# Kernel optimization log

Hardware: AMD Instinct MI355X
Metric: run time of the kernel (lower is better)

Reference implementation:

```python
import jax, jax.numpy as jnp
import numpy as np

N = 100000        # nodes
E = 1600000       # directed edges (before self loops)
F = 128           # input node features
H1, H2, H3 = 64, 32, 16
G = 64            # graphs in batch
EPS = 1e-5
NEG_SLOPE = 0.2


def setup_inputs():
    key = jax.random.key(0)
    ks = jax.random.split(key, 16)
    def rn(k, shape, scale=1.0):
        return jax.random.normal(k, shape, dtype=jnp.float32) * scale
    inp = {}
    inp['x'] = rn(ks[0], (N, F))
    inp['edge_index'] = jax.random.randint(ks[1], (2, E), 0, N)
    inp['batch'] = jnp.sort(jax.random.randint(ks[2], (N,), 0, G))
    dims = [(F, H1), (H1, H2), (H2, H3)]
    i = 3
    for li, (fi, fo) in enumerate(dims, start=1):
        s = 1.0 / np.sqrt(fi)
        kk = jax.random.split(ks[i], 3)
        inp[f'Wl{li}'] = rn(kk[0], (fi, fo), s)
        inp[f'bl{li}'] = jnp.zeros((fo,), jnp.float32)
        inp[f'Wr{li}'] = rn(kk[1], (fi, fo), s)
        inp[f'br{li}'] = jnp.zeros((fo,), jnp.float32)
        inp[f'att{li}'] = rn(kk[2], (fo,), 1.0 / np.sqrt(fo))
        inp[f'bias{li}'] = jnp.zeros((fo,), jnp.float32)
        inp[f'gamma{li}'] = jnp.ones((fo,), jnp.float32)
        inp[f'beta{li}'] = jnp.zeros((fo,), jnp.float32)
        i += 1
    inp['linW'] = rn(ks[i], (H3, 1), 0.25)
    inp['linb'] = jnp.zeros((1,), jnp.float32)
    return inp


def _gatv2(x, Wl, bl, Wr, br, att, bias, src, dst):
    # PyG GATv2Conv, heads=1: e_ij = a^T LeakyReLU(Wl x_j + Wr x_i)
    xl = x @ Wl + bl                         # [N, H] source transform
    xr = x @ Wr + br                         # [N, H] target transform
    e = jax.nn.leaky_relu(xl[src] + xr[dst], NEG_SLOPE) @ att   # [E']
    # numerically stable segment softmax over incoming edges of dst
    emax = jax.ops.segment_max(e, dst, num_segments=N)
    w = jnp.exp(e - emax[dst])
    denom = jax.ops.segment_sum(w, dst, num_segments=N)
    alpha = w / (denom[dst] + 1e-16)         # [E']
    out = jax.ops.segment_sum(alpha[:, None] * xl[src], dst, num_segments=N)
    return out + bias


def _batchnorm(x, gamma, beta):
    mu = jnp.mean(x, axis=0)
    var = jnp.var(x, axis=0)
    return (x - mu) * jax.lax.rsqrt(var + EPS) * gamma + beta


def reference(x, edge_index, batch,
              Wl1, bl1, Wr1, br1, att1, bias1, gamma1, beta1,
              Wl2, bl2, Wr2, br2, att2, bias2, gamma2, beta2,
              Wl3, bl3, Wr3, br3, att3, bias3, gamma3, beta3,
              linW, linb):
    # add self loops once (PyG GATv2Conv default add_self_loops=True)
    loops = jnp.arange(N, dtype=edge_index.dtype)
    src = jnp.concatenate([edge_index[0], loops])
    dst = jnp.concatenate([edge_index[1], loops])

    h = _gatv2(x, Wl1, bl1, Wr1, br1, att1, bias1, src, dst)
    h = jax.nn.relu(_batchnorm(h, gamma1, beta1))
    h = _gatv2(h, Wl2, bl2, Wr2, br2, att2, bias2, src, dst)
    h = jax.nn.relu(_batchnorm(h, gamma2, beta2))
    h = _gatv2(h, Wl3, bl3, Wr3, br3, att3, bias3, src, dst)
    h = jax.nn.relu(_batchnorm(h, gamma3, beta3))

    # global mean pool over graphs
    sums = jax.ops.segment_sum(h, batch, num_segments=G)          # [G, 16]
    cnts = jax.ops.segment_sum(jnp.ones((N,), h.dtype), batch, num_segments=G)
    pooled = sums / jnp.maximum(cnts, 1.0)[:, None]
    return pooled @ linW + linb                                   # [G, 1]
```

## Files before the change

### kernel.cpp

```cpp
#include <hip/hip_runtime.h>
#include <hip/hip_bf16.h>


static constexpr int G_ = 64;

typedef short bfrag __attribute__((ext_vector_type(8)));
typedef float facc  __attribute__((ext_vector_type(4)));

__device__ __forceinline__ float bf2f(unsigned short u) {
  union { unsigned int i; float f; } c;
  c.i = ((unsigned int)u) << 16;
  return c.f;
}
__device__ __forceinline__ unsigned short f2bf(float f) {
  union { float f; unsigned int i; } c;
  c.f = f;
  unsigned int r = c.i + 0x7FFFu + ((c.i >> 16) & 1u);
  return (unsigned short)(r >> 16);
}

__global__ __launch_bounds__(256) void pack_all(
    const float* __restrict__ Wl1, const float* __restrict__ Wr1,
    const float* __restrict__ bl1, const float* __restrict__ br1,
    const float* __restrict__ Wl2, const float* __restrict__ Wr2,
    const float* __restrict__ bl2, const float* __restrict__ br2,
    const float* __restrict__ Wl3, const float* __restrict__ Wr3,
    const float* __restrict__ bl3, const float* __restrict__ br3,
    unsigned short* __restrict__ Wt1, float* __restrict__ bc1,
    unsigned short* __restrict__ Wt2, float* __restrict__ bc2,
    unsigned short* __restrict__ Wt3, float* __restrict__ bc3) {
  int i = blockIdx.x * 256 + threadIdx.x;
  if (i < 128 * 128) { int c = i >> 7, k = i & 127;
    Wt1[i] = f2bf((c < 64) ? Wl1[k * 64 + c] : Wr1[k * 64 + (c - 64)]); }
  if (i < 128) bc1[i] = (i < 64) ? bl1[i] : br1[i - 64];
  if (i < 64 * 64) { int c = i >> 6, k = i & 63;
    Wt2[i] = f2bf((c < 32) ? Wl2[k * 32 + c] : Wr2[k * 32 + (c - 32)]); }
  if (i < 64) bc2[i] = (i < 32) ? bl2[i] : br2[i - 32];
  if (i < 32 * 32) { int c = i >> 5, k = i & 31;
    Wt3[i] = f2bf((c < 16) ? Wl3[k * 16 + c] : Wr3[k * 16 + (c - 16)]); }
  if (i < 32) bc3[i] = (i < 16) ? bl3[i] : br3[i - 16];
}

__global__ __launch_bounds__(256) void edge_hist(
    const int* __restrict__ ei, int* __restrict__ deg, int E, int Etot, int N) {
  int p = blockIdx.x & 7;
  int q = blockIdx.x >> 3;
  int nbq = gridDim.x >> 3;
  float scale = 8.0f / (float)N;
  for (int i = q * 256 + threadIdx.x; i < Etot; i += nbq * 256) {
    int dst = (i < E) ? ei[E + i] : (i - E);
    int pp = min((int)((float)dst * scale), 7);
    if (pp == p) atomicAdd(&deg[dst], 1);
  }
}

__global__ __launch_bounds__(256) void scan1(
    const int* __restrict__ deg, int* __restrict__ part, int* __restrict__ bsums, int n) {
  __shared__ int ts[256];
  int t = threadIdx.x, b = blockIdx.x;
  int base = b * 1024 + t * 4;
  int d[4];
#pragma unroll
  for (int q = 0; q < 4; q++) d[q] = (base + q < n) ? deg[base + q] : 0;
  int s = d[0] + d[1] + d[2] + d[3];
  ts[t] = s;
  __syncthreads();
  for (int o = 1; o < 256; o <<= 1) {
    int v = (t >= o) ? ts[t - o] : 0;
    __syncthreads();
    ts[t] += v;
    __syncthreads();
  }
  int incl = ts[t];
  if (t == 255) bsums[b] = incl;
  int run = incl - s;
#pragma unroll
  for (int q = 0; q < 4; q++) {
    if (base + q < n) part[base + q] = run;
    run += d[q];
  }
}

__global__ void scan2(int* bsums, int nb) {
  __shared__ int s[256];
  int t = threadIdx.x;
  int v = (t < nb) ? bsums[t] : 0;
  s[t] = v;
  __syncthreads();
  for (int o = 1; o < 256; o <<= 1) {
    int u = (t >= o) ? s[t - o] : 0;
    __syncthreads();
    s[t] += u;
    __syncthreads();
  }
  if (t < nb) bsums[t] = s[t] - v;
}

__global__ __launch_bounds__(256) void scan3(
    int* __restrict__ rp, int* __restrict__ cur, const int* __restrict__ bsums,
    int n, int Etot) {
  int i = blockIdx.x * 256 + threadIdx.x;
  if (i < n) {
    int v = rp[i] + bsums[i >> 10];
    rp[i] = v; cur[i] = v;
  }
  if (i == 0) rp[n] = Etot;
}

__global__ __launch_bounds__(256) void scatter_edges(
    const int* __restrict__ ei, int* __restrict__ cur, int* __restrict__ ssrc,
    int E, int Etot, int N) {
  int p = blockIdx.x & 7;
  int q = blockIdx.x >> 3;
  int nbq = gridDim.x >> 3;
  float scale = 8.0f / (float)N;
  for (int i = q * 256 + threadIdx.x; i < Etot; i += nbq * 256) {
    int dst = (i < E) ? ei[E + i] : (i - E);
    int pp = min((int)((float)dst * scale), 7);
    if (pp != p) continue;
    int src = (i < E) ? ei[i] : (i - E);
    int pos = atomicAdd(&cur[dst], 1);
    ssrc[pos] = src;
  }
}

template <int FI, int FO, bool AFP32>
__global__ __launch_bounds__(256) void gemm_mfma(
    const void* __restrict__ Ain, const unsigned short* __restrict__ Wt,
    const float* __restrict__ bcat, unsigned short* __restrict__ Cb, int N) {
  constexpr int NT = FO / 16;
  constexpr int KS = FI / 32;
  int tid = threadIdx.x;
  int w = tid >> 6;
  int lr = tid & 15;
  int lg = (tid & 63) >> 4;
  int n0 = blockIdx.x * 64;
  int arow = min(n0 + w * 16 + lr, N - 1);

  facc acc[NT];
#pragma unroll
  for (int t = 0; t < NT; t++)
#pragma unroll
    for (int e = 0; e < 4; e++) acc[t][e] = 0.f;

#pragma unroll
  for (int ks = 0; ks < KS; ks++) {
    int k0 = ks * 32 + lg * 8;
    bfrag a;
    if constexpr (AFP32) {
      const float* Af = (const float*)Ain;
      const float* p = &Af[(size_t)arow * FI + k0];
      float4 lo = *reinterpret_cast<const float4*>(p);
      float4 hi = *reinterpret_cast<const float4*>(p + 4);
      union { bfrag v; unsigned short u[8]; } cv;
      cv.u[0] = f2bf(lo.x); cv.u[1] = f2bf(lo.y);
      cv.u[2] = f2bf(lo.z); cv.u[3] = f2bf(lo.w);
      cv.u[4] = f2bf(hi.x); cv.u[5] = f2bf(hi.y);
      cv.u[6] = f2bf(hi.z); cv.u[7] = f2bf(hi.w);
      a = cv.v;
    } else {
      const unsigned short* Ab = (const unsigned short*)Ain;
      a = *reinterpret_cast<const bfrag*>(&Ab[(size_t)arow * FI + k0]);
    }
#pragma unroll
    for (int t = 0; t < NT; t++) {
      bfrag b = *reinterpret_cast<const bfrag*>(&Wt[(size_t)(t * 16 + lr) * FI + k0]);
      acc[t] = __builtin_amdgcn_mfma_f32_16x16x32_bf16(a, b, acc[t], 0, 0, 0);
    }
  }

#pragma unroll
  for (int t = 0; t < NT; t++) {
    int col = t * 16 + lr;
    float bias = bcat[col];
#pragma unroll
    for (int r = 0; r < 4; r++) {
      int n = n0 + w * 16 + lg * 4 + r;
      if (n < N) Cb[(size_t)n * FO + col] = f2bf(acc[t][r] + bias);
    }
  }
}

__device__ __forceinline__ float lrelu02(float z) {
  return (z > 0.f) ? z : 0.2f * z;
}

template <int H, bool UN2>
__global__ __launch_bounds__(256) void gat_agg2(
    const unsigned short* __restrict__ xlr, const float* __restrict__ att,
    const float* __restrict__ bias, const int* __restrict__ rp,
    const int* __restrict__ ssrc, float* __restrict__ out, int N) {
  constexpr int L = H / 4;
  constexpr int C = 64 / L;
  int v = blockIdx.x * 4 + (threadIdx.x >> 6);
  if (v >= N) return;
  int lane = threadIdx.x & 63;
  int fl = lane % L;
  int sub = lane / L;

  ushort4 qr = *reinterpret_cast<const ushort4*>(&xlr[(size_t)v * (2 * H) + H + fl * 4]);
  float xr0 = bf2f(qr.x), xr1 = bf2f(qr.y), xr2 = bf2f(qr.z), xr3 = bf2f(qr.w);
  const float4 a4 = *reinterpret_cast<const float4*>(&att[fl * 4]);
  int beg = rp[v], end = rp[v + 1];

  float mA = -3.0e38f, dA = 0.f;
  float4 accA = make_float4(0.f, 0.f, 0.f, 0.f);
  float mB = -3.0e38f, dB = 0.f;
  float4 accB = make_float4(0.f, 0.f, 0.f, 0.f);

  constexpr int STEP = UN2 ? 2 * C : C;

  for (int j = beg + sub; j < end; j += STEP) {
    {
      int u = ssrc[j];
      ushort4 q = *reinterpret_cast<const ushort4*>(&xlr[(size_t)u * (2 * H) + fl * 4]);
      float x0 = bf2f(q.x), x1 = bf2f(q.y), x2 = bf2f(q.z), x3 = bf2f(q.w);
      float t = a4.x * lrelu02(x0 + xr0);
      t = fmaf(a4.y, lrelu02(x1 + xr1), t);
      t = fmaf(a4.z, lrelu02(x2 + xr2), t);
      t = fmaf(a4.w, lrelu02(x3 + xr3), t);
#pragma unroll
      for (int o = L / 2; o >= 1; o >>= 1) t += __shfl_xor(t, o);
      float diff = t - mA;
      if (diff > 8.f) {
        float sc = __expf(-diff);
        dA *= sc;
        accA.x *= sc; accA.y *= sc; accA.z *= sc; accA.w *= sc;
        mA = t; diff = 0.f;
      }
      float w = __expf(diff);
      dA += w;
      accA.x = fmaf(w, x0, accA.x);
      accA.y = fmaf(w, x1, accA.y);
      accA.z = fmaf(w, x2, accA.z);
      accA.w = fmaf(w, x3, accA.w);
    }
    if (UN2) {
      int j2 = j + C;
      if (j2 < end) {
        int u = ssrc[j2];
        ushort4 q = *reinterpret_cast<const ushort4*>(&xlr[(size_t)u * (2 * H) + fl * 4]);
        float x0 = bf2f(q.x), x1 = bf2f(q.y), x2 = bf2f(q.z), x3 = bf2f(q.w);
        float t = a4.x * lrelu02(x0 + xr0);
        t = fmaf(a4.y, lrelu02(x1 + xr1), t);
        t = fmaf(a4.z, lrelu02(x2 + xr2), t);
        t = fmaf(a4.w, lrelu02(x3 + xr3), t);
#pragma unroll
        for (int o = L / 2; o >= 1; o >>= 1) t += __shfl_xor(t, o);
        float diff = t - mB;
        if (diff > 8.f) {
          float sc = __expf(-diff);
          dB *= sc;
          accB.x *= sc; accB.y *= sc; accB.z *= sc; accB.w *= sc;
          mB = t; diff = 0.f;
        }
        float w = __expf(diff);
        dB += w;
        accB.x = fmaf(w, x0, accB.x);
        accB.y = fmaf(w, x1, accB.y);
        accB.z = fmaf(w, x2, accB.z);
        accB.w = fmaf(w, x3, accB.w);
      }
    }
  }

  if (UN2) {
    float mn = fmaxf(mA, mB);
    float s1 = __expf(mA - mn), s2 = __expf(mB - mn);
    dA = dA * s1 + dB * s2;
    accA.x = accA.x * s1 + accB.x * s2;
    accA.y = accA.y * s1 + accB.y * s2;
    accA.z = accA.z * s1 + accB.z * s2;
    accA.w = accA.w * s1 + accB.w * s2;
    mA = mn;
  }

#pragma unroll
  for (int o = L; o < 64; o <<= 1) {
    float mo = __shfl_xor(mA, o);
    float d2 = __shfl_xor(dA, o);
    float ax = __shfl_xor(accA.x, o);
    float ay = __shfl_xor(accA.y, o);
    float az = __shfl_xor(accA.z, o);
    float aw = __shfl_xor(accA.w, o);
    float mn = fmaxf(mA, mo);
    float s1 = __expf(mA - mn), s2 = __expf(mo - mn);
    dA = dA * s1 + d2 * s2;
    accA.x = accA.x * s1 + ax * s2;
    accA.y = accA.y * s1 + ay * s2;
    accA.z = accA.z * s1 + az * s2;
    accA.w = accA.w * s1 + aw * s2;
    mA = mn;
  }

  if (lane < L) {
    float inv = 1.f / (dA + 1e-16f);
    const float4 b4 = *reinterpret_cast<const float4*>(&bias[fl * 4]);
    float4 o4 = make_float4(fmaf(accA.x, inv, b4.x), fmaf(accA.y, inv, b4.y),
                            fmaf(accA.z, inv, b4.z), fmaf(accA.w, inv, b4.w));
    *reinterpret_cast<float4*>(&out[(size_t)v * H + fl * 4]) = o4;
  }
}

template <int H>
__global__ __launch_bounds__(256) void bn_stats(
    const float* __restrict__ X, float* __restrict__ stats, int N) {
  __shared__ float ls[256], ls2[256];
  int tid = threadIdx.x;
  int h = tid % H;
  constexpr int RPB = 256 / H;
  int r0 = blockIdx.x * RPB + tid / H;
  float s = 0.f, s2 = 0.f;
  for (int n = r0; n < N; n += gridDim.x * RPB) {
    float val = X[(size_t)n * H + h];
    s += val; s2 += val * val;
  }
  ls[tid] = s; ls2[tid] = s2;
  __syncthreads();
  if (tid < H) {
    for (int g = 1; g < RPB; g++) { s += ls[tid + g * H]; s2 += ls2[tid + g * H]; }
    atomicAdd(&stats[h], s);
    atomicAdd(&stats[H + h], s2);
  }
}

__global__ void bn_finalize(
    const float* __restrict__ stats, const float* __restrict__ gamma,
    const float* __restrict__ beta, float* __restrict__ ss, int H, int N) {
  int h = threadIdx.x;
  if (h < H) {
    float mean = stats[h] / (float)N;
    float var = stats[H + h] / (float)N - mean * mean;
    float istd = rsqrtf(var + 1e-5f);
    float sc = gamma[h] * istd;
    ss[h] = sc;
    ss[H + h] = beta[h] - mean * sc;
  }
}

template <int H>
__global__ __launch_bounds__(256) void bn_apply_b16(
    const float* __restrict__ X, const float* __restrict__ ss,
    unsigned short* __restrict__ Y, int N) {
  int g = blockIdx.x * 256 + threadIdx.x;
  if (g >= N * (H / 4)) return;
  int i = g * 4;
  int h = i & (H - 1);
  float4 v = *reinterpret_cast<const float4*>(&X[i]);
  float t0 = fmaxf(fmaf(v.x, ss[h + 0], ss[H + h + 0]), 0.f);
  float t1 = fmaxf(fmaf(v.y, ss[h + 1], ss[H + h + 1]), 0.f);
  float t2 = fmaxf(fmaf(v.z, ss[h + 2], ss[H + h + 2]), 0.f);
  float t3 = fmaxf(fmaf(v.w, ss[h + 3], ss[H + h + 3]), 0.f);
  uint2 o;
  o.x = (unsigned)f2bf(t0) | ((unsigned)f2bf(t1) << 16);
  o.y = (unsigned)f2bf(t2) | ((unsigned)f2bf(t3) << 16);
  *reinterpret_cast<uint2*>(&Y[i]) = o;
}

__global__ __launch_bounds__(256) void pool_kernel(
    const float* __restrict__ X, const float* __restrict__ ss,
    const int* __restrict__ batch, float* __restrict__ pool,
    float* __restrict__ cnt, int N) {
  __shared__ float lp[G_ * 16];
  __shared__ float lc[G_];
  int tid = threadIdx.x;
  for (int j = tid; j < G_ * 16; j += 256) lp[j] = 0.f;
  if (tid < G_) lc[tid] = 0.f;
  __syncthreads();
  int tot = N * 16;
  for (int i = blockIdx.x * 256 + tid; i < tot; i += gridDim.x * 256) {
    int n = i >> 4, h = i & 15;
    int g = batch[n];
    float t = X[i] * ss[h] + ss[16 + h];
    t = (t > 0.f) ? t : 0.f;
    atomicAdd(&lp[g * 16 + h], t);
    if (h == 0) atomicAdd(&lc[g], 1.0f);
  }
  __syncthreads();
  for (int j = tid; j < G_ * 16; j += 256) atomicAdd(&pool[j], lp[j]);
  if (tid < G_) atomicAdd(&cnt[tid], lc[tid]);
}

__global__ void final_linear(
    const float* __restrict__ pool, const float* __restrict__ cnt,
    const float* __restrict__ linW, const float* __restrict__ linb,
    float* __restrict__ out) {
  int g = threadIdx.x;
  if (g < G_) {
    float c = fmaxf(cnt[g], 1.0f);
    float acc = 0.f;
    for (int h = 0; h < 16; h++) acc += (pool[g * 16 + h] / c) * linW[h];
    out[g] = acc + linb[0];
  }
}

extern "C" void kernel_launch(void* const* d_in, const int* in_sizes, int n_in,
                              void* d_out, int out_size, void* d_ws, size_t ws_size,
                              hipStream_t stream) {
  const float* x = (const float*)d_in[0];
  const int* ei = (const int*)d_in[1];
  const int* batch = (const int*)d_in[2];
  const int N = in_sizes[0] / 128;
  const int E = in_sizes[1] / 2;
  const int Etot = E + N;

  char* wsb = (char*)d_ws;
  size_t off = 0;
  auto alloc = [&](size_t bytes) -> void* {
    void* p = wsb + off;
    off += (bytes + 255) & ~(size_t)255;
    return p;
  };
  unsigned short* R1b = (unsigned short*)alloc((size_t)128 * N * 2);
  float* R2 = (float*)alloc((size_t)64 * N * 4);
  unsigned short* hb = (unsigned short*)alloc((size_t)64 * N * 2);
  int* row_ptr = (int*)alloc((size_t)(N + 1) * 4);
  int* cursor = (int*)alloc((size_t)N * 4);
  int* bsums = (int*)alloc(4096);
  int* ssrc = (int*)alloc((size_t)Etot * 4);
  unsigned short* Wt1 = (unsigned short*)alloc(16384 * 2);
  float* bc1 = (float*)alloc(128 * 4);
  unsigned short* Wt2 = (unsigned short*)alloc(4096 * 2);
  float* bc2 = (float*)alloc(64 * 4);
  unsigned short* Wt3 = (unsigned short*)alloc(1024 * 2);
  float* bc3 = (float*)alloc(32 * 4);
  float* ss = (float*)alloc(128 * 4);
  size_t zelems = (size_t)N + 3 * 128 + G_ * 16 + G_;
  char* zb = (char*)alloc(zelems * 4);
  int* deg = (int*)zb;
  float* stats1 = (float*)(zb + (size_t)N * 4);
  float* stats2 = stats1 + 128;
  float* stats3 = stats2 + 128;
  float* pool = stats3 + 128;
  float* cnt = pool + G_ * 16;

  const float* Wl1 = (const float*)d_in[3];  const float* bl1 = (const float*)d_in[4];
  const float* Wr1 = (const float*)d_in[5];  const float* br1 = (const float*)d_in[6];
  const float* att1 = (const float*)d_in[7]; const float* bias1 = (const float*)d_in[8];
  const float* g1 = (const float*)d_in[9];   const float* b1 = (const float*)d_in[10];
  const float* Wl2 = (const float*)d_in[11]; const float* bl2 = (const float*)d_in[12];
  const float* Wr2 = (const float*)d_in[13]; const float* br2 = (const float*)d_in[14];
  const float* att2 = (const float*)d_in[15]; const float* bias2 = (const float*)d_in[16];
  const float* g2 = (const float*)d_in[17];  const float* b2 = (const float*)d_in[18];
  const float* Wl3 = (const float*)d_in[19]; const float* bl3 = (const float*)d_in[20];
  const float* Wr3 = (const float*)d_in[21]; const float* br3 = (const float*)d_in[22];
  const float* att3 = (const float*)d_in[23]; const float* bias3 = (const float*)d_in[24];
  const float* g3 = (const float*)d_in[25];  const float* b3 = (const float*)d_in[26];
  const float* linW = (const float*)d_in[27]; const float* linb = (const float*)d_in[28];
  float* out = (float*)d_out;

  int nb = (N + 1023) / 1024;
  int nnodeblk = (N + 3) / 4;
  int ngemm = (N + 63) / 64;

  pack_all<<<64, 256, 0, stream>>>(Wl1, Wr1, bl1, br1, Wl2, Wr2, bl2, br2,
                                   Wl3, Wr3, bl3, br3, Wt1, bc1, Wt2, bc2, Wt3, bc3);
  hipMemsetAsync(zb, 0, zelems * 4, stream);

  edge_hist<<<4096, 256, 0, stream>>>(ei, deg, E, Etot, N);
  scan1<<<nb, 256, 0, stream>>>(deg, row_ptr, bsums, N);
  scan2<<<1, 256, 0, stream>>>(bsums, nb);
  scan3<<<(N + 255) / 256, 256, 0, stream>>>(row_ptr, cursor, bsums, N, Etot);
  scatter_edges<<<4096, 256, 0, stream>>>(ei, cursor, ssrc, E, Etot, N);

  gemm_mfma<128, 128, true><<<ngemm, 256, 0, stream>>>(x, Wt1, bc1, R1b, N);
  gat_agg2<64, true><<<nnodeblk, 256, 0, stream>>>(R1b, att1, bias1, row_ptr, ssrc, R2, N);
  bn_stats<64><<<512, 256, 0, stream>>>(R2, stats1, N);
  bn_finalize<<<1, 64, 0, stream>>>(stats1, g1, b1, ss, 64, N);
  bn_apply_b16<64><<<(N * 16 + 255) / 256, 256, 0, stream>>>(R2, ss, hb, N);

  gemm_mfma<64, 64, false><<<ngemm, 256, 0, stream>>>(hb, Wt2, bc2, R1b, N);
  gat_agg2<32, true><<<nnodeblk, 256, 0, stream>>>(R1b, att2, bias2, row_ptr, ssrc, R2, N);
  bn_stats<32><<<512, 256, 0, stream>>>(R2, stats2, N);
  bn_finalize<<<1, 64, 0, stream>>>(stats2, g2, b2, ss, 32, N);
  bn_apply_b16<32><<<(N * 8 + 255) / 256, 256, 0, stream>>>(R2, ss, hb, N);

  gemm_mfma<32, 32, false><<<ngemm, 256, 0, stream>>>(hb, Wt3, bc3, R1b, N);
  gat_agg2<16, false><<<nnodeblk, 256, 0, stream>>>(R1b, att3, bias3, row_ptr, ssrc, R2, N);
  bn_stats<16><<<512, 256, 0, stream>>>(R2, stats3, N);
  bn_finalize<<<1, 64, 0, stream>>>(stats3, g3, b3, ss, 16, N);

  pool_kernel<<<2048, 256, 0, stream>>>(R2, ss, batch, pool, cnt, N);
  final_linear<<<1, 64, 0, stream>>>(pool, cnt, linW, linb, out);
}
```

Measured before the change: 518.4 us.

## Fuse BN-apply into next GEMM and widen per-lane features in GAT aggregation

Removes the separate bn_apply_b16 kernels. The next layer's GEMM now reads the fp32 aggregation output directly and applies the BN scale/shift plus ReLU before converting to bf16, which saves one kernel launch and an extra write/read of activations per layer. The GAT aggregation is generalised so each lane handles 8 features for layers 1 and 2 instead of 4. That means fewer lanes per edge, more edges in flight per wavefront and shorter shuffle reductions, at the cost of more registers per lane. The GEMM A-load now reads fp32 instead of bf16 for layers 2 and 3, doubling the bytes of that input.

New measurement: 538.8 us. +3.9%, slower.

```diff
diff --git a/kernel.cpp b/kernel.cpp
--- a/kernel.cpp
+++ b/kernel.cpp
@@ -7,16 +7,32 @@
 typedef short bfrag __attribute__((ext_vector_type(8)));
 typedef float facc  __attribute__((ext_vector_type(4)));
 
+__device__ __forceinline__ float asfloat_(unsigned int u) {
+  union { unsigned int i; float f; } c; c.i = u; return c.f;
+}
 __device__ __forceinline__ float bf2f(unsigned short u) {
-  union { unsigned int i; float f; } c;
-  c.i = ((unsigned int)u) << 16;
-  return c.f;
+  return asfloat_(((unsigned int)u) << 16);
 }
 __device__ __forceinline__ unsigned short f2bf(float f) {
   union { float f; unsigned int i; } c;
   c.f = f;
   unsigned int r = c.i + 0x7FFFu + ((c.i >> 16) & 1u);
   return (unsigned short)(r >> 16);
+}
+
+template <int FPL>
+__device__ __forceinline__ void load_bf(const unsigned short* p, float* f) {
+  if constexpr (FPL == 8) {
+    uint4 q = *reinterpret_cast<const uint4*>(p);
+    f[0] = asfloat_(q.x << 16); f[1] = asfloat_(q.x & 0xFFFF0000u);
+    f[2] = asfloat_(q.y << 16); f[3] = asfloat_(q.y & 0xFFFF0000u);
+    f[4] = asfloat_(q.z << 16); f[5] = asfloat_(q.z & 0xFFFF0000u);
+    f[6] = asfloat_(q.w << 16); f[7] = asfloat_(q.w & 0xFFFF0000u);
+  } else {
+    uint2 q = *reinterpret_cast<const uint2*>(p);
+    f[0] = asfloat_(q.x << 16); f[1] = asfloat_(q.x & 0xFFFF0000u);
+    f[2] = asfloat_(q.y << 16); f[3] = asfloat_(q.y & 0xFFFF0000u);
+  }
 }
 
 __global__ __launch_bounds__(256) void pack_all(
@@ -124,10 +140,11 @@
   }
 }
 
-template <int FI, int FO, bool AFP32>
+template <int FI, int FO, int AMODE>
 __global__ __launch_bounds__(256) void gemm_mfma(
-    const void* __restrict__ Ain, const unsigned short* __restrict__ Wt,
-    const float* __restrict__ bcat, unsigned short* __restrict__ Cb, int N) {
+    const void* __restrict__ Ain, const float* __restrict__ ssb,
+    const unsigned short* __restrict__ Wt, const float* __restrict__ bcat,
+    unsigned short* __restrict__ Cb, int N) {
   constexpr int NT = FO / 16;
   constexpr int KS = FI / 32;
   int tid = threadIdx.x;
@@ -147,20 +164,29 @@
   for (int ks = 0; ks < KS; ks++) {
     int k0 = ks * 32 + lg * 8;
     bfrag a;
-    if constexpr (AFP32) {
+    if constexpr (AMODE == 0) {
+      const unsigned short* Ab = (const unsigned short*)Ain;
+      a = *reinterpret_cast<const bfrag*>(&Ab[(size_t)arow * FI + k0]);
+    } else {
       const float* Af = (const float*)Ain;
       const float* p = &Af[(size_t)arow * FI + k0];
       float4 lo = *reinterpret_cast<const float4*>(p);
       float4 hi = *reinterpret_cast<const float4*>(p + 4);
+      float f[8] = {lo.x, lo.y, lo.z, lo.w, hi.x, hi.y, hi.z, hi.w};
+      if constexpr (AMODE == 2) {
+        float4 sc0 = *reinterpret_cast<const float4*>(&ssb[k0]);
+        float4 sc1 = *reinterpret_cast<const float4*>(&ssb[k0 + 4]);
+        float4 sh0 = *reinterpret_cast<const float4*>(&ssb[FI + k0]);
+        float4 sh1 = *reinterpret_cast<const float4*>(&ssb[FI + k0 + 4]);
+        float sc[8] = {sc0.x, sc0.y, sc0.z, sc0.w, sc1.x, sc1.y, sc1.z, sc1.w};
+        float sh[8] = {sh0.x, sh0.y, sh0.z, sh0.w, sh1.x, sh1.y, sh1.z, sh1.w};
+#pragma unroll
+        for (int e = 0; e < 8; e++) f[e] = fmaxf(fmaf(f[e], sc[e], sh[e]), 0.f);
+      }
       union { bfrag v; unsigned short u[8]; } cv;
-      cv.u[0] = f2bf(lo.x); cv.u[1] = f2bf(lo.y);
-      cv.u[2] = f2bf(lo.z); cv.u[3] = f2bf(lo.w);
-      cv.u[4] = f2bf(hi.x); cv.u[5] = f2bf(hi.y);
-      cv.u[6] = f2bf(hi.z); cv.u[7] = f2bf(hi.w);
+#pragma unroll
+      for (int e = 0; e < 8; e++) cv.u[e] = f2bf(f[e]);
       a = cv.v;
-    } else {
-      const unsigned short* Ab = (const unsigned short*)Ain;
-      a = *reinterpret_cast<const bfrag*>(&Ab[(size_t)arow * FI + k0]);
     }
 #pragma unroll
     for (int t = 0; t < NT; t++) {
@@ -182,85 +208,65 @@
 }
 
 __device__ __forceinline__ float lrelu02(float z) {
-  return (z > 0.f) ? z : 0.2f * z;
-}
-
-template <int H, bool UN2>
-__global__ __launch_bounds__(256) void gat_agg2(
+  return fmaxf(z, 0.2f * z);
+}
+
+template <int H, int FPL, bool UN2>
+__global__ __launch_bounds__(256) void gat_agg3(
     const unsigned short* __restrict__ xlr, const float* __restrict__ att,
     const float* __restrict__ bias, const int* __restrict__ rp,
     const int* __restrict__ ssrc, float* __restrict__ out, int N) {
-  constexpr int L = H / 4;
+  constexpr int L = H / FPL;
   constexpr int C = 64 / L;
+  constexpr int STEP = UN2 ? 2 * C : C;
   int v = blockIdx.x * 4 + (threadIdx.x >> 6);
   if (v >= N) return;
   int lane = threadIdx.x & 63;
   int fl = lane % L;
   int sub = lane / L;
 
-  ushort4 qr = *reinterpret_cast<const ushort4*>(&xlr[(size_t)v * (2 * H) + H + fl * 4]);
-  float xr0 = bf2f(qr.x), xr1 = bf2f(qr.y), xr2 = bf2f(qr.z), xr3 = bf2f(qr.w);
-  const float4 a4 = *reinterpret_cast<const float4*>(&att[fl * 4]);
+  float xr[FPL], a[FPL];
+  load_bf<FPL>(&xlr[(size_t)v * (2 * H) + H + fl * FPL], xr);
+#pragma unroll
+  for (int e = 0; e < FPL; e += 4) {
+    float4 av = *reinterpret_cast<const float4*>(&att[fl * FPL + e]);
+    a[e] = av.x; a[e + 1] = av.y; a[e + 2] = av.z; a[e + 3] = av.w;
+  }
   int beg = rp[v], end = rp[v + 1];
 
-  float mA = -3.0e38f, dA = 0.f;
-  float4 accA = make_float4(0.f, 0.f, 0.f, 0.f);
-  float mB = -3.0e38f, dB = 0.f;
-  float4 accB = make_float4(0.f, 0.f, 0.f, 0.f);
-
-  constexpr int STEP = UN2 ? 2 * C : C;
+  float mA = -3.0e38f, dA = 0.f, accA[FPL];
+  float mB = -3.0e38f, dB = 0.f, accB[FPL];
+#pragma unroll
+  for (int e = 0; e < FPL; e++) { accA[e] = 0.f; accB[e] = 0.f; }
+
+  auto edge = [&](int j, float& m, float& d, float (&acc)[FPL]) {
+    int u = ssrc[j];
+    float xl[FPL];
+    load_bf<FPL>(&xlr[(size_t)u * (2 * H) + fl * FPL], xl);
+    float t = 0.f;
+#pragma unroll
+    for (int e = 0; e < FPL; e++) t = fmaf(a[e], lrelu02(xl[e] + xr[e]), t);
+#pragma unroll
+    for (int o = L / 2; o >= 1; o >>= 1) t += __shfl_xor(t, o);
+    float diff = t - m;
+    if (diff > 8.f) {
+      float sc = __expf(-diff);
+      d *= sc;
+#pragma unroll
+      for (int e = 0; e < FPL; e++) acc[e] *= sc;
+      m = t; diff = 0.f;
+    }
+    float w = __expf(diff);
+    d += w;
+#pragma unroll
+    for (int e = 0; e < FPL; e++) acc[e] = fmaf(w, xl[e], acc[e]);
+  };
 
   for (int j = beg + sub; j < end; j += STEP) {
-    {
-      int u = ssrc[j];
-      ushort4 q = *reinterpret_cast<const ushort4*>(&xlr[(size_t)u * (2 * H) + fl * 4]);
-      float x0 = bf2f(q.x), x1 = bf2f(q.y), x2 = bf2f(q.z), x3 = bf2f(q.w);
-      float t = a4.x * lrelu02(x0 + xr0);
-      t = fmaf(a4.y, lrelu02(x1 + xr1), t);
-      t = fmaf(a4.z, lrelu02(x2 + xr2), t);
-      t = fmaf(a4.w, lrelu02(x3 + xr3), t);
-#pragma unroll
-      for (int o = L / 2; o >= 1; o >>= 1) t += __shfl_xor(t, o);
-      float diff = t - mA;
-      if (diff > 8.f) {
-        float sc = __expf(-diff);
-        dA *= sc;
-        accA.x *= sc; accA.y *= sc; accA.z *= sc; accA.w *= sc;
-        mA = t; diff = 0.f;
-      }
-      float w = __expf(diff);
-      dA += w;
-      accA.x = fmaf(w, x0, accA.x);
-      accA.y = fmaf(w, x1, accA.y);
-      accA.z = fmaf(w, x2, accA.z);
-      accA.w = fmaf(w, x3, accA.w);
-    }
+    edge(j, mA, dA, accA);
     if (UN2) {
       int j2 = j + C;
-      if (j2 < end) {
-        int u = ssrc[j2];
-        ushort4 q = *reinterpret_cast<const ushort4*>(&xlr[(size_t)u * (2 * H) + fl * 4]);
-        float x0 = bf2f(q.x), x1 = bf2f(q.y), x2 = bf2f(q.z), x3 = bf2f(q.w);
-        float t = a4.x * lrelu02(x0 + xr0);
-        t = fmaf(a4.y, lrelu02(x1 + xr1), t);
-        t = fmaf(a4.z, lrelu02(x2 + xr2), t);
-        t = fmaf(a4.w, lrelu02(x3 + xr3), t);
-#pragma unroll
-        for (int o = L / 2; o >= 1; o >>= 1) t += __shfl_xor(t, o);
-        float diff = t - mB;
-        if (diff > 8.f) {
-          float sc = __expf(-diff);
-          dB *= sc;
-          accB.x *= sc; accB.y *= sc; accB.z *= sc; accB.w *= sc;
-          mB = t; diff = 0.f;
-        }
-        float w = __expf(diff);
-        dB += w;
-        accB.x = fmaf(w, x0, accB.x);
-        accB.y = fmaf(w, x1, accB.y);
-        accB.z = fmaf(w, x2, accB.z);
-        accB.w = fmaf(w, x3, accB.w);
-      }
+      if (j2 < end) edge(j2, mB, dB, accB);
     }
   }
 
@@ -268,10 +274,8 @@
     float mn = fmaxf(mA, mB);
     float s1 = __expf(mA - mn), s2 = __expf(mB - mn);
     dA = dA * s1 + dB * s2;
-    accA.x = accA.x * s1 + accB.x * s2;
-    accA.y = accA.y * s1 + accB.y * s2;
-    accA.z = accA.z * s1 + accB.z * s2;
-    accA.w = accA.w * s1 + accB.w * s2;
+#pragma unroll
+    for (int e = 0; e < FPL; e++) accA[e] = accA[e] * s1 + accB[e] * s2;
     mA = mn;
   }
 
@@ -279,26 +283,28 @@
   for (int o = L; o < 64; o <<= 1) {
     float mo = __shfl_xor(mA, o);
     float d2 = __shfl_xor(dA, o);
-    float ax = __shfl_xor(accA.x, o);
-    float ay = __shfl_xor(accA.y, o);
-    float az = __shfl_xor(accA.z, o);
-    float aw = __shfl_xor(accA.w, o);
+    float ao[FPL];
+#pragma unroll
+    for (int e = 0; e < FPL; e++) ao[e] = __shfl_xor(accA[e], o);
     float mn = fmaxf(mA, mo);
     float s1 = __expf(mA - mn), s2 = __expf(mo - mn);
     dA = dA * s1 + d2 * s2;
-    accA.x = accA.x * s1 + ax * s2;
-    accA.y = accA.y * s1 + ay * s2;
-    accA.z = accA.z * s1 + az * s2;
-    accA.w = accA.w * s1 + aw * s2;
+#pragma unroll
+    for (int e = 0; e < FPL; e++) accA[e] = accA[e] * s1 + ao[e] * s2;
     mA = mn;
   }
 
   if (lane < L) {
     float inv = 1.f / (dA + 1e-16f);
-    const float4 b4 = *reinterpret_cast<const float4*>(&bias[fl * 4]);
-    float4 o4 = make_float4(fmaf(accA.x, inv, b4.x), fmaf(accA.y, inv, b4.y),
-                            fmaf(accA.z, inv, b4.z), fmaf(accA.w, inv, b4.w));
-    *reinterpret_cast<float4*>(&out[(size_t)v * H + fl * 4]) = o4;
+#pragma unroll
+    for (int e = 0; e < FPL; e += 4) {
+      float4 b4 = *reinterpret_cast<const float4*>(&bias[fl * FPL + e]);
+      float4 o4 = make_float4(fmaf(accA[e + 0], inv, b4.x),
+                              fmaf(accA[e + 1], inv, b4.y),
+                              fmaf(accA[e + 2], inv, b4.z),
+                              fmaf(accA[e + 3], inv, b4.w));
+      *reinterpret_cast<float4*>(&out[(size_t)v * H + fl * FPL + e]) = o4;
+    }
   }
 }
 
@@ -336,25 +342,6 @@
     ss[h] = sc;
     ss[H + h] = beta[h] - mean * sc;
   }
-}
-
-template <int H>
-__global__ __launch_bounds__(256) void bn_apply_b16(
-    const float* __restrict__ X, const float* __restrict__ ss,
-    unsigned short* __restrict__ Y, int N) {
-  int g = blockIdx.x * 256 + threadIdx.x;
-  if (g >= N * (H / 4)) return;
-  int i = g * 4;
-  int h = i & (H - 1);
-  float4 v = *reinterpret_cast<const float4*>(&X[i]);
-  float t0 = fmaxf(fmaf(v.x, ss[h + 0], ss[H + h + 0]), 0.f);
-  float t1 = fmaxf(fmaf(v.y, ss[h + 1], ss[H + h + 1]), 0.f);
-  float t2 = fmaxf(fmaf(v.z, ss[h + 2], ss[H + h + 2]), 0.f);
-  float t3 = fmaxf(fmaf(v.w, ss[h + 3], ss[H + h + 3]), 0.f);
-  uint2 o;
-  o.x = (unsigned)f2bf(t0) | ((unsigned)f2bf(t1) << 16);
-  o.y = (unsigned)f2bf(t2) | ((unsigned)f2bf(t3) << 16);
-  *reinterpret_cast<uint2*>(&Y[i]) = o;
 }
 
 __global__ __launch_bounds__(256) void pool_kernel(
@@ -413,7 +400,6 @@
   };
   unsigned short* R1b = (unsigned short*)alloc((size_t)128 * N * 2);
   float* R2 = (float*)alloc((size_t)64 * N * 4);
-  unsigned short* hb = (unsigned short*)alloc((size_t)64 * N * 2);
   int* row_ptr = (int*)alloc((size_t)(N + 1) * 4);
   int* cursor = (int*)alloc((size_t)N * 4);
   int* bsums = (int*)alloc(4096);
@@ -424,7 +410,7 @@
   float* bc2 = (float*)alloc(64 * 4);
   unsigned short* Wt3 = (unsigned short*)alloc(1024 * 2);
   float* bc3 = (float*)alloc(32 * 4);
-  float* ss = (float*)alloc(128 * 4);
+  float* ss = (float*)alloc(256 * 4);
   size_t zelems = (size_t)N + 3 * 128 + G_ * 16 + G_;
   char* zb = (char*)alloc(zelems * 4);
   int* deg = (int*)zb;
@@ -463,20 +449,18 @@
   scan3<<<(N + 255) / 256, 256, 0, stream>>>(row_ptr, cursor, bsums, N, Etot);
   scatter_edges<<<4096, 256, 0, stream>>>(ei, cursor, ssrc, E, Etot, N);
 
-  gemm_mfma<128, 128, true><<<ngemm, 256, 0, stream>>>(x, Wt1, bc1, R1b, N);
-  gat_agg2<64, true><<<nnodeblk, 256, 0, stream>>>(R1b, att1, bias1, row_ptr, ssrc, R2, N);
+  gemm_mfma<128, 128, 1><<<ngemm, 256, 0, stream>>>(x, nullptr, Wt1, bc1, R1b, N);
+  gat_agg3<64, 8, true><<<nnodeblk, 256, 0, stream>>>(R1b, att1, bias1, row_ptr, ssrc, R2, N);
   bn_stats<64><<<512, 256, 0, stream>>>(R2, stats1, N);
   bn_finalize<<<1, 64, 0, stream>>>(stats1, g1, b1, ss, 64, N);
-  bn_apply_b16<64><<<(N * 16 + 255) / 256, 256, 0, stream>>>(R2, ss, hb, N);
-
-  gemm_mfma<64, 64, false><<<ngemm, 256, 0, stream>>>(hb, Wt2, bc2, R1b, N);
-  gat_agg2<32, true><<<nnodeblk, 256, 0, stream>>>(R1b, att2, bias2, row_ptr, ssrc, R2, N);
+
+  gemm_mfma<64, 64, 2><<<ngemm, 256, 0, stream>>>(R2, ss, Wt2, bc2, R1b, N);
+  gat_agg3<32, 8, true><<<nnodeblk, 256, 0, stream>>>(R1b, att2, bias2, row_ptr, ssrc, R2, N);
   bn_stats<32><<<512, 256, 0, stream>>>(R2, stats2, N);
   bn_finalize<<<1, 64, 0, stream>>>(stats2, g2, b2, ss, 32, N);
-  bn_apply_b16<32><<<(N * 8 + 255) / 256, 256, 0, stream>>>(R2, ss, hb, N);
-
-  gemm_mfma<32, 32, false><<<ngemm, 256, 0, stream>>>(hb, Wt3, bc3, R1b, N);
-  gat_agg2<16, false><<<nnodeblk, 256, 0, stream>>>(R1b, att3, bias3, row_ptr, ssrc, R2, N);
+
+  gemm_mfma<32, 32, 2><<<ngemm, 256, 0, stream>>>(R2, ss, Wt3, bc3, R1b, N);
+  gat_agg3<16, 4, false><<<nnodeblk, 256, 0, stream>>>(R1b, att3, bias3, row_ptr, ssrc, R2, N);
   bn_stats<16><<<512, 256, 0, stream>>>(R2, stats3, N);
   bn_finalize<<<1, 64, 0, stream>>>(stats3, g3, b3, ss, 16, N);
 
```
